# Optimization experiments

Hardware: AMD Instinct MI355X
Metric: run time of the kernel (lower is better)

Reference implementation:

```python
import jax, jax.numpy as jnp
import numpy as np

B, L, DM = 32, 64, 512
NODES = 16            # patch_size -> graph nodes
NODE_DIM = 10
CONV_CH, SKIP_CH = 32, 32
GDEP = 2
ALPHA = 0.05
D_STATE, D_CONV = 16, 4
D_INNER = 2 * DM      # Mamba expand=2
DT_RANK = DM // 16    # 32
K = DM - NODES + 1    # start_conv kernel height = 497


def setup_inputs() -> dict:
    key = jax.random.key(0)
    ks = jax.random.split(key, 16)
    n = jax.random.normal
    inp = {
        "x": n(ks[0], (B, L, DM), jnp.float32),
        "nodevec1": n(ks[1], (NODES, NODE_DIM), jnp.float32),
        "nodevec2": n(ks[2], (NODE_DIM, NODES), jnp.float32),
        "start_w": n(ks[3], (CONV_CH, K), jnp.float32) * 0.02,
        "start_b": jnp.zeros((CONV_CH,), jnp.float32),
        "mix_w": n(ks[4], (SKIP_CH, (GDEP + 1) * CONV_CH), jnp.float32) * 0.05,
        "mix_b": jnp.zeros((SKIP_CH,), jnp.float32),
        "end_w": n(ks[5], (L, SKIP_CH, L), jnp.float32) * 0.02,
        "end_b": jnp.zeros((L,), jnp.float32),
        "lin_w": n(ks[6], (DM, NODES), jnp.float32) * 0.05,
        "lin_b": jnp.zeros((DM,), jnp.float32),
        "gnorm_g": jnp.ones((DM,), jnp.float32),
        "gnorm_b": jnp.zeros((DM,), jnp.float32),
        "in_proj_w": n(ks[7], (2 * D_INNER, DM), jnp.float32) * 0.02,
        "conv_w": n(ks[8], (D_INNER, D_CONV), jnp.float32) * 0.2,
        "conv_b": jnp.zeros((D_INNER,), jnp.float32),
        "xproj_w": n(ks[9], (DT_RANK + 2 * D_STATE, D_INNER), jnp.float32) * 0.02,
        "dtproj_w": n(ks[10], (D_INNER, DT_RANK), jnp.float32) * 0.05,
        "dtproj_b": n(ks[11], (D_INNER,), jnp.float32) * 0.05,
        "A_log": jnp.log(jnp.tile(jnp.arange(1, D_STATE + 1, dtype=jnp.float32), (D_INNER, 1))),
        "Dp": jnp.ones((D_INNER,), jnp.float32),
        "out_proj_w": n(ks[12], (DM, D_INNER), jnp.float32) * 0.02,
        "norm_g": jnp.ones((DM,), jnp.float32),
        "norm_b": jnp.zeros((DM,), jnp.float32),
    }
    return inp


def layer_norm(x, g, b, eps=1e-5):
    mu = x.mean(-1, keepdims=True)
    var = ((x - mu) ** 2).mean(-1, keepdims=True)
    return (x - mu) / jnp.sqrt(var + eps) * g + b


def graph_block(x, nodevec1, nodevec2, start_w, start_b, mix_w, mix_b,
                end_w, end_b, lin_w, lin_b, gnorm_g, gnorm_b):
    # adaptive adjacency over the NODES=16 graph nodes
    adp = jax.nn.softmax(jax.nn.relu(nodevec1 @ nodevec2), axis=1)
    # start_conv: Conv2d(1, CONV_CH, (DM-NODES+1, 1)) on [B,1,DM,L]
    xi = jnp.swapaxes(x, 1, 2)  # [B, DM, L]
    windows = jnp.stack([xi[:, i:i + K, :] for i in range(NODES)], axis=1)  # [B, NODES, K, L]
    h0 = jnp.einsum('bikl,ck->bcil', windows, start_w) + start_b[None, :, None, None]  # [B,CONV_CH,NODES,L]
    # mixprop graph conv
    adj = adp + jnp.eye(NODES, dtype=x.dtype)
    a = adj / adj.sum(axis=1, keepdims=True)
    h = h0
    outs = [h]
    for _ in range(GDEP):
        h = ALPHA * h0 + (1.0 - ALPHA) * jnp.einsum('bcwl,vw->bcvl', h, a)
        outs.append(h)
    ho = jnp.concatenate(outs, axis=1)  # [B, (GDEP+1)*CONV_CH, NODES, L]
    ho = jnp.einsum('bcil,oc->boil', ho, mix_w) + mix_b[None, :, None, None]  # 1x1 conv mlp
    ho = jax.nn.gelu(ho, approximate=False)
    # end_conv: Conv2d(SKIP_CH, L, (1, L)) -> [B, L, NODES]
    out = jnp.einsum('bcil,ocl->boi', ho, end_w) + end_b[None, :, None]
    out = out @ lin_w.T + lin_b  # [B, L, DM]
    return layer_norm(x + out, gnorm_g, gnorm_b)


def mamba(x, in_proj_w, conv_w, conv_b, xproj_w, dtproj_w, dtproj_b,
          A_log, Dp, out_proj_w):
    xz = x @ in_proj_w.T                       # [B,L,2*D_INNER]
    xin, z = jnp.split(xz, 2, axis=-1)
    # causal depthwise conv1d
    xt = jnp.swapaxes(xin, 1, 2)               # [B, D_INNER, L]
    xp = jnp.pad(xt, ((0, 0), (0, 0), (D_CONV - 1, 0)))
    xc = sum(xp[:, :, k:k + L] * conv_w[None, :, k, None] for k in range(D_CONV))
    xc = xc + conv_b[None, :, None]
    xc = jax.nn.silu(jnp.swapaxes(xc, 1, 2))   # [B, L, D_INNER]
    x_dbl = xc @ xproj_w.T
    dt, Bm, Cm = jnp.split(x_dbl, [DT_RANK, DT_RANK + D_STATE], axis=-1)
    dt = jax.nn.softplus(dt @ dtproj_w.T + dtproj_b)      # [B,L,D_INNER]
    A = -jnp.exp(A_log)                                    # [D_INNER, D_STATE]
    dA = jnp.exp(dt[..., None] * A)                        # [B,L,D_INNER,D_STATE]
    dBu = dt[..., None] * Bm[:, :, None, :] * xc[..., None]

    def step(h, inputs):
        dA_t, dBu_t, C_t = inputs
        h = dA_t * h + dBu_t                               # [B,D_INNER,D_STATE]
        y = jnp.einsum('bds,bs->bd', h, C_t)
        return h, y

    h0 = jnp.zeros((B, D_INNER, D_STATE), dtype=x.dtype)
    _, ys = jax.lax.scan(step, h0, (jnp.swapaxes(dA, 0, 1),
                                    jnp.swapaxes(dBu, 0, 1),
                                    jnp.swapaxes(Cm, 0, 1)))
    y = jnp.swapaxes(ys, 0, 1) + xc * Dp                   # skip term D*u
    y = y * jax.nn.silu(z)
    return y @ out_proj_w.T


def reference(x, nodevec1, nodevec2, start_w, start_b, mix_w, mix_b, end_w, end_b,
              lin_w, lin_b, gnorm_g, gnorm_b, in_proj_w, conv_w, conv_b, xproj_w,
              dtproj_w, dtproj_b, A_log, Dp, out_proj_w, norm_g, norm_b):
    xg = graph_block(x, nodevec1, nodevec2, start_w, start_b, mix_w, mix_b,
                     end_w, end_b, lin_w, lin_b, gnorm_g, gnorm_b)
    out = layer_norm(mamba(xg, in_proj_w, conv_w, conv_b, xproj_w, dtproj_w,
                           dtproj_b, A_log, Dp, out_proj_w), norm_g, norm_b)
    out = jax.nn.gelu(out, approximate=False)
    return out + xg
```

## Files before the change

### kernel.cpp

```cpp
#include <hip/hip_runtime.h>
#include <hip/hip_bf16.h>
#include <math.h>

typedef __hip_bfloat16 bf16;
typedef __attribute__((ext_vector_type(8))) short short8;
typedef __attribute__((ext_vector_type(4))) float f32x4;

#define B_ 32
#define L_ 64
#define DM_ 512
#define NODES_ 16
#define KW_ 497
#define DIN_ 1024

__device__ __forceinline__ float b2f(bf16 x){ return __bfloat162float(x); }
__device__ __forceinline__ bf16 f2b(float x){ return __float2bfloat16(x); }
__device__ __forceinline__ float us2f(unsigned short u){ return __uint_as_float(((unsigned)u)<<16); }
__device__ __forceinline__ float geluf(float x){ return 0.5f*x*(1.0f+erff(x*0.70710678118654752f)); }
__device__ __forceinline__ float siluf(float x){ return x/(1.0f+__expf(-x)); }

__global__ void __launch_bounds__(256) k_prep(const float* ew, bf16* ewt, const float* win, bf16* wbin,
                       const float* wo, bf16* wob, const float* xw, bf16* xwb,
                       const float* dw, float* dwt, const float* x, bf16* xbf,
                       const float* sw, bf16* SwT,
                       const float* nv1, const float* nv2,
                       const float* mw, const float* mb, const float* sb,
                       bf16* Q, float* bcomp){
  int bid = blockIdx.x;
  int tid = threadIdx.x;
  if (bid < 512){
    int idx = bid*256 + tid;
    int o = idx >> 11, j = idx & 2047;
    int c = j & 31, l = j >> 5;
    ewt[idx] = f2b(ew[o*2048 + c*64 + l]);
  } else if (bid < 4608){
    int idx = (bid-512)*256 + tid;
    wbin[idx] = f2b(win[idx]);
  } else if (bid < 6656){
    int idx = (bid-4608)*256 + tid;
    wob[idx] = f2b(wo[idx]);
  } else if (bid < 6912){
    int idx = (bid-6656)*256 + tid;
    xwb[idx] = f2b(xw[idx]);
  } else if (bid < 7040){
    int k = (bid-6912)*256 + tid;
    dwt[k] = dw[(k & 1023)*32 + (k >> 10)];
  } else if (bid < 11136){
    int idx = (bid-7040)*256 + tid;
    xbf[idx] = f2b(x[idx]);
  } else if (bid < 12160){
    int idx = (bid-11136)*256 + tid;
    int k = idx >> 9, m = idx & 511;
    int c = m >> 4, w = m & 15;
    int kk = k - w;
    SwT[idx] = f2b((kk >= 0 && kk < KW_) ? sw[c*KW_ + kk] : 0.f);
  } else {
    __shared__ float as[256], M1[256], M2[256], mws[32*96], sbs[32], bo[32];
    int qb = bid - 12160;
    for (int t=tid; t<32*96; t+=256) mws[t]=mw[t];
    if (tid<32) sbs[tid]=sb[tid];
    __syncthreads();
    if (tid<16){
      int i=tid;
      float row[16];
      for(int j=0;j<16;j++){ float s=0.f; for(int k=0;k<10;k++) s+=nv1[i*10+k]*nv2[k*16+j]; row[j]=fmaxf(s,0.f); }
      float m=row[0]; for(int j=1;j<16;j++) m=fmaxf(m,row[j]);
      float den=0.f; for(int j=0;j<16;j++){row[j]=__expf(row[j]-m); den+=row[j];}
      for(int j=0;j<16;j++) row[j]/=den;
      row[i]+=1.f;
      float rs=0.f; for(int j=0;j<16;j++) rs+=row[j];
      float inv=1.f/rs;
      for(int j=0;j<16;j++) as[i*16+j]=row[j]*inv;
    }
    __syncthreads();
    { int i=tid>>4, w=tid&15;
      M1[tid] = 0.05f*((i==w)?1.f:0.f) + 0.95f*as[i*16+w]; }
    __syncthreads();
    { int i=tid>>4, w=tid&15;
      float s=0.f;
      for(int u=0;u<16;u++) s+=as[i*16+u]*M1[u*16+w];
      M2[tid] = 0.05f*((i==w)?1.f:0.f) + 0.95f*s; }
    if (tid<32){
      float s=mb[tid];
      for(int c=0;c<32;c++) s += (mws[tid*96+c]+mws[tid*96+32+c]+mws[tid*96+64+c])*sbs[c];
      bo[tid]=s;
    }
    __syncthreads();
    if (qb == 0){
      for (int n=tid; n<512; n+=256) bcomp[n] = bo[n&31];
    }
    int base = qb*4096;
    for (int t=tid; t<4096; t+=256){
      int idx = base + t;
      int n=idx>>9, m=idx&511;
      int i=n>>5, o=n&31, c=m>>4, w=m&15;
      float v = mws[o*96+c]*((i==w)?1.f:0.f)
              + mws[o*96+32+c]*M1[i*16+w]
              + mws[o*96+64+c]*M2[i*16+w];
      Q[idx]=f2b(v);
    }
  }
}

__global__ void __launch_bounds__(256) k_gemmU(const ushort* A, int lda,
                                               const ushort* W, int ldw,
                                               int K, bf16* C, int ldc,
                                               const float* bias, int act){
  __shared__ ushort As[128*56] __attribute__((aligned(16)));
  __shared__ ushort Ws[128*56] __attribute__((aligned(16)));
  int tid = threadIdx.x;
  int m0 = blockIdx.y*128, n0 = blockIdx.x*128;
  int lane = tid & 63, wave = tid >> 6;
  int wm = (wave>>1)*64, wn = (wave&1)*64;
  int l15 = lane & 15, quad = lane >> 4;
  f32x4 acc[4][4];
  #pragma unroll
  for (int mi=0;mi<4;mi++)
    #pragma unroll
    for (int ni=0;ni<4;ni++) acc[mi][ni] = (f32x4){0.f,0.f,0.f,0.f};
  for (int k0 = 0; k0 < K; k0 += 32){
    __syncthreads();
    #pragma unroll
    for (int p=0;p<2;p++){
      int idx = p*256 + tid;
      int row = idx>>2, ch = idx&3;
      *(uint4*)&As[row*56 + ch*8] = *(const uint4*)(A + (size_t)(m0+row)*lda + k0 + ch*8);
      *(uint4*)&Ws[row*56 + ch*8] = *(const uint4*)(W + (size_t)(n0+row)*ldw + k0 + ch*8);
    }
    __syncthreads();
    short8 af[4], bfr[4];
    #pragma unroll
    for (int mi=0;mi<4;mi++) af[mi] = *(const short8*)&As[(wm+mi*16+l15)*56 + quad*8];
    #pragma unroll
    for (int ni=0;ni<4;ni++) bfr[ni] = *(const short8*)&Ws[(wn+ni*16+l15)*56 + quad*8];
    #pragma unroll
    for (int mi=0;mi<4;mi++)
      #pragma unroll
      for (int ni=0;ni<4;ni++)
        acc[mi][ni] = __builtin_amdgcn_mfma_f32_16x16x32_bf16(af[mi], bfr[ni], acc[mi][ni], 0, 0, 0);
  }
  #pragma unroll
  for (int mi=0;mi<4;mi++){
    #pragma unroll
    for (int ni=0;ni<4;ni++){
      int col = n0 + wn + ni*16 + l15;
      float bs = (act==1) ? bias[col] : 0.f;
      #pragma unroll
      for (int r=0;r<4;r++){
        int row = m0 + wm + mi*16 + quad*4 + r;
        float v = acc[mi][ni][r];
        if (act==1) v = geluf(v + bs);
        C[(size_t)row*ldc + col] = f2b(v);
      }
    }
  }
}

__global__ void __launch_bounds__(256) k_gemmC(const ushort* A, const ushort* W,
                                               const float* cw, const float* cb,
                                               bf16* xcb, bf16* zb){
  __shared__ ushort smem[16896] __attribute__((aligned(16)));
  ushort* As = smem;
  ushort* Ws = smem + 7168;
  int tid = threadIdx.x;
  int m0 = blockIdx.y*128, n0 = blockIdx.x*128;
  int lane = tid & 63, wave = tid >> 6;
  int wm = (wave>>1)*64, wn = (wave&1)*64;
  int l15 = lane & 15, quad = lane >> 4;
  f32x4 acc[4][4];
  #pragma unroll
  for (int mi=0;mi<4;mi++)
    #pragma unroll
    for (int ni=0;ni<4;ni++) acc[mi][ni] = (f32x4){0.f,0.f,0.f,0.f};
  for (int k0 = 0; k0 < 512; k0 += 32){
    __syncthreads();
    #pragma unroll
    for (int p=0;p<2;p++){
      int idx = p*256 + tid;
      int row = idx>>2, ch = idx&3;
      *(uint4*)&As[row*56 + ch*8] = *(const uint4*)(A + (size_t)(m0+row)*512 + k0 + ch*8);
      *(uint4*)&Ws[row*56 + ch*8] = *(const uint4*)(W + (size_t)(n0+row)*512 + k0 + ch*8);
    }
    __syncthreads();
    short8 af[4], bfr[4];
    #pragma unroll
    for (int mi=0;mi<4;mi++) af[mi] = *(const short8*)&As[(wm+mi*16+l15)*56 + quad*8];
    #pragma unroll
    for (int ni=0;ni<4;ni++) bfr[ni] = *(const short8*)&Ws[(wn+ni*16+l15)*56 + quad*8];
    #pragma unroll
    for (int mi=0;mi<4;mi++)
      #pragma unroll
      for (int ni=0;ni<4;ni++)
        acc[mi][ni] = __builtin_amdgcn_mfma_f32_16x16x32_bf16(af[mi], bfr[ni], acc[mi][ni], 0, 0, 0);
  }
  if (n0 >= 1024){
    #pragma unroll
    for (int mi=0;mi<4;mi++){
      #pragma unroll
      for (int ni=0;ni<4;ni++){
        int col = n0 - 1024 + wn + ni*16 + l15;
        #pragma unroll
        for (int r=0;r<4;r++){
          int row = m0 + wm + mi*16 + quad*4 + r;
          zb[(size_t)row*1024 + col] = f2b(acc[mi][ni][r]);
        }
      }
    }
    return;
  }
  __syncthreads();
  ushort* st = smem + wave*4224;
  #pragma unroll
  for (int mi=0;mi<4;mi++){
    #pragma unroll
    for (int ni=0;ni<4;ni++){
      #pragma unroll
      for (int r=0;r<4;r++){
        bf16 v = f2b(acc[mi][ni][r]);
        st[(mi*16+quad*4+r)*66 + ni*16+l15] = *(unsigned short*)&v;
      }
    }
  }
  __syncthreads();
  int j = n0 + wn + lane;
  float w0 = cw[j*4+0], w1 = cw[j*4+1], w2 = cw[j*4+2], w3 = cw[j*4+3];
  float cbj = cb[j];
  float p0=0.f, p1=0.f, p2=0.f;
  int rowbase = m0 + wm;
  for (int rr=0; rr<64; rr++){
    float xv = us2f(st[rr*66 + lane]);
    float v = cbj + w0*p0 + w1*p1 + w2*p2 + w3*xv;
    xcb[(size_t)(rowbase+rr)*1024 + j] = f2b(siluf(v));
    p0 = p1; p1 = p2; p2 = xv;
  }
}

__global__ void __launch_bounds__(256) k_xprojM(const ushort* A, const ushort* W,
                                                float* xdl, float* BC){
  __shared__ ushort As[64*56] __attribute__((aligned(16)));
  __shared__ ushort Ws[64*56] __attribute__((aligned(16)));
  int tid = threadIdx.x;
  int m0 = blockIdx.y*64;
  int lane = tid & 63, wave = tid >> 6;
  int wm = (wave>>1)*32, wn = (wave&1)*32;
  int l15 = lane & 15, quad = lane >> 4;
  f32x4 acc[2][2];
  #pragma unroll
  for (int mi=0;mi<2;mi++)
    #pragma unroll
    for (int ni=0;ni<2;ni++) acc[mi][ni] = (f32x4){0.f,0.f,0.f,0.f};
  for (int k0 = 0; k0 < 1024; k0 += 32){
    __syncthreads();
    int row = tid>>2, ch = tid&3;
    *(uint4*)&As[row*56 + ch*8] = *(const uint4*)(A + (size_t)(m0+row)*1024 + k0 + ch*8);
    *(uint4*)&Ws[row*56 + ch*8] = *(const uint4*)(W + (size_t)row*1024 + k0 + ch*8);
    __syncthreads();
    short8 af[2], bfr[2];
    #pragma unroll
    for (int mi=0;mi<2;mi++) af[mi] = *(const short8*)&As[(wm+mi*16+l15)*56 + quad*8];
    #pragma unroll
    for (int ni=0;ni<2;ni++) bfr[ni] = *(const short8*)&Ws[(wn+ni*16+l15)*56 + quad*8];
    #pragma unroll
    for (int mi=0;mi<2;mi++)
      #pragma unroll
      for (int ni=0;ni<2;ni++)
        acc[mi][ni] = __builtin_amdgcn_mfma_f32_16x16x32_bf16(af[mi], bfr[ni], acc[mi][ni], 0, 0, 0);
  }
  #pragma unroll
  for (int mi=0;mi<2;mi++){
    #pragma unroll
    for (int ni=0;ni<2;ni++){
      int col = wn + ni*16 + l15;
      #pragma unroll
      for (int r=0;r<4;r++){
        int row = m0 + wm + mi*16 + quad*4 + r;
        float v = acc[mi][ni][r];
        if (col < 32) xdl[row*32 + col] = v;
        else          BC[row*32 + (col-32)] = v;
      }
    }
  }
}

__global__ void k_endconv(const bf16* mixed, const bf16* ewt, const float* eb, float* eout){
  __shared__ float ms[2048];
  __shared__ float psum[64][4];
  int bi = blockIdx.x;
  int b = bi >> 4, i = bi & 15;
  int tid = threadIdx.x;
  {
    int t0 = tid*8;
    int l = t0 >> 5, cc0 = t0 & 31;
    short8 v = *(const short8*)(mixed + (size_t)(b*64+l)*512 + i*32 + cc0);
    #pragma unroll
    for (int k=0;k<8;k++) ms[t0+k] = us2f((unsigned short)v[k]);
  }
  __syncthreads();
  int o = tid >> 2, q = tid & 3;
  const short8* er8 = (const short8*)(ewt + (size_t)o*2048 + q*512);
  const float* mr = ms + q*512;
  float p0 = 0.f, p1 = 0.f;
  for (int j8=0;j8<64;j8++){
    short8 w8 = er8[j8];
    const float* mq = mr + j8*8;
    p0 += mq[0]*us2f((unsigned short)w8[0]) + mq[1]*us2f((unsigned short)w8[1])
        + mq[2]*us2f((unsigned short)w8[2]) + mq[3]*us2f((unsigned short)w8[3]);
    p1 += mq[4]*us2f((unsigned short)w8[4]) + mq[5]*us2f((unsigned short)w8[5])
        + mq[6]*us2f((unsigned short)w8[6]) + mq[7]*us2f((unsigned short)w8[7]);
  }
  psum[o][q] = p0 + p1;
  __syncthreads();
  if (tid < 64){
    float s = psum[tid][0]+psum[tid][1]+psum[tid][2]+psum[tid][3] + eb[tid];
    eout[(b*64+tid)*16 + i] = s;
  }
}

__global__ void __launch_bounds__(512) k_linln(const float* eout, const float* x, const float* lw, const float* lb,
                        const float* gg, const float* gb, bf16* xgb){
  __shared__ float es[16];
  __shared__ float red[8];
  int tok = blockIdx.x;
  int tid = threadIdx.x;
  if (tid < 16) es[tid] = eout[tok*16 + tid];
  __syncthreads();
  float v = x[tok*512+tid] + lb[tid];
  for (int i=0;i<16;i++) v += es[i]*lw[tid*16+i];
  float s = v;
  for (int off=32; off; off>>=1) s += __shfl_down(s, off, 64);
  int wv = tid>>6, ln = tid&63;
  if (ln==0) red[wv] = s;
  __syncthreads();
  if (tid==0){ float t=0.f; for(int w=0;w<8;w++) t+=red[w]; red[0]=t; }
  __syncthreads();
  float mean = red[0] * (1.f/512.f);
  __syncthreads();
  float d = v - mean;
  float s2 = d*d;
  for (int off=32; off; off>>=1) s2 += __shfl_down(s2, off, 64);
  if (ln==0) red[wv] = s2;
  __syncthreads();
  if (tid==0){ float t=0.f; for(int w=0;w<8;w++) t+=red[w]; red[0]=t; }
  __syncthreads();
  float rstd = rsqrtf(red[0]*(1.f/512.f) + 1e-5f);
  xgb[tok*512+tid] = f2b(d*rstd*gg[tid] + gb[tid]);
}

__global__ void __launch_bounds__(256) k_gemm64(const ushort* A, int lda,
                                                const ushort* W, int ldw,
                                                int K, char* Cb){
  __shared__ ushort As[64*56] __attribute__((aligned(16)));
  __shared__ ushort Ws[64*56] __attribute__((aligned(16)));
  int tid = threadIdx.x;
  int m0 = blockIdx.y*64, n0 = blockIdx.x*64;
  int lane = tid & 63, wave = tid >> 6;
  int wm = (wave>>1)*32, wn = (wave&1)*32;
  int l15 = lane & 15, quad = lane >> 4;
  f32x4 acc[2][2];
  #pragma unroll
  for (int mi=0;mi<2;mi++)
    #pragma unroll
    for (int ni=0;ni<2;ni++) acc[mi][ni] = (f32x4){0.f,0.f,0.f,0.f};
  for (int k0 = 0; k0 < K; k0 += 32){
    __syncthreads();
    int row = tid>>2, ch = tid&3;
    *(uint4*)&As[row*56 + ch*8] = *(const uint4*)(A + (size_t)(m0+row)*lda + k0 + ch*8);
    *(uint4*)&Ws[row*56 + ch*8] = *(const uint4*)(W + (size_t)(n0+row)*ldw + k0 + ch*8);
    __syncthreads();
    short8 af[2], bfr[2];
    #pragma unroll
    for (int mi=0;mi<2;mi++) af[mi] = *(const short8*)&As[(wm+mi*16+l15)*56 + quad*8];
    #pragma unroll
    for (int ni=0;ni<2;ni++) bfr[ni] = *(const short8*)&Ws[(wn+ni*16+l15)*56 + quad*8];
    #pragma unroll
    for (int mi=0;mi<2;mi++)
      #pragma unroll
      for (int ni=0;ni<2;ni++)
        acc[mi][ni] = __builtin_amdgcn_mfma_f32_16x16x32_bf16(af[mi], bfr[ni], acc[mi][ni], 0, 0, 0);
  }
  #pragma unroll
  for (int mi=0;mi<2;mi++){
    #pragma unroll
    for (int ni=0;ni<2;ni++){
      int col = n0 + wn + ni*16 + l15;
      #pragma unroll
      for (int r=0;r<4;r++){
        int row = m0 + wm + mi*16 + quad*4 + r;
        *(float*)(Cb + (size_t)row*4096 + col*4) = acc[mi][ni][r];
      }
    }
  }
}

__global__ void __launch_bounds__(128) k_scan5(const float* xdl, const float* BCg,
                       const float* dwt, const float* db, const float* Dp,
                       const bf16* zb, bf16* xcb){
  __shared__ float bcs[2048];
  __shared__ float xds[2048];
  __shared__ unsigned short xcl[8192];
  __shared__ unsigned short zl[8192];
  int tid = threadIdx.x;
  int b = blockIdx.x >> 3, q = blockIdx.x & 7;
  int d = q*128 + tid;
  for (int t=tid; t<2048; t+=128){ bcs[t] = BCg[b*2048+t]; xds[t] = xdl[b*2048+t]; }
  for (int t=tid; t<8192; t+=128){
    int l = t >> 7, dl = t & 127;
    xcl[t] = ((const unsigned short*)xcb)[(size_t)(b*64+l)*1024 + q*128 + dl];
    zl[t]  = ((const unsigned short*)zb)[(size_t)(b*64+l)*1024 + q*128 + dl];
  }
  float myw[32];
  #pragma unroll
  for (int qq=0;qq<32;qq++) myw[qq] = dwt[qq*1024 + d];
  float dbv = db[d];
  float Dd = Dp[d];
  __syncthreads();
  float h[16];
  #pragma unroll
  for (int s=0;s<16;s++) h[s]=0.f;
  for (int l=0;l<64;l++){
    const float* xr = xds + l*32;
    float a0=dbv, a1=0.f, a2=0.f, a3=0.f;
    #pragma unroll
    for (int j=0;j<8;j++){
      a0 += xr[j]     *myw[j];
      a1 += xr[8+j]   *myw[8+j];
      a2 += xr[16+j]  *myw[16+j];
      a3 += xr[24+j]  *myw[24+j];
    }
    float dtv = (a0+a1)+(a2+a3);
    if (dtv <= 20.f) dtv = __logf(1.f + __expf(dtv));
    float xcv = us2f(xcl[l*128 + tid]);
    float dx = dtv*xcv;
    float e1 = __expf(-dtv);
    float e2 = e1*e1, e4 = e2*e2, e8 = e4*e4;
    float dA[16];
    dA[0]=e1;       dA[1]=e2;       dA[2]=e2*e1;     dA[3]=e4;
    dA[4]=e4*e1;    dA[5]=e4*e2;    dA[6]=e4*dA[2];  dA[7]=e8;
    dA[8]=e8*e1;    dA[9]=e8*e2;    dA[10]=e8*dA[2]; dA[11]=e8*e4;
    dA[12]=e8*dA[4];dA[13]=e8*dA[5];dA[14]=e8*dA[6]; dA[15]=e8*e8;
    const float* bl = bcs + l*32;
    float y0=0.f,y1=0.f,y2=0.f,y3=0.f;
    #pragma unroll
    for (int s=0;s<16;s+=4){
      h[s]   = dA[s]  *h[s]   + dx*bl[s];    y0 += h[s]  *bl[16+s];
      h[s+1] = dA[s+1]*h[s+1] + dx*bl[s+1];  y1 += h[s+1]*bl[17+s];
      h[s+2] = dA[s+2]*h[s+2] + dx*bl[s+2];  y2 += h[s+2]*bl[18+s];
      h[s+3] = dA[s+3]*h[s+3] + dx*bl[s+3];  y3 += h[s+3]*bl[19+s];
    }
    float y = (y0+y1)+(y2+y3);
    float zv = us2f(zl[l*128 + tid]);
    xcb[(size_t)(b*64+l)*1024 + d] = f2b((y + xcv*Dd) * siluf(zv));
  }
}

__global__ void __launch_bounds__(512) k_outfin(const char* ypb, const bf16* xgb,
                        const float* ng, const float* nb, float* out){
  __shared__ float red[8];
  int tok = blockIdx.x, tid = threadIdx.x;
  const float* yr = (const float*)(ypb + (size_t)tok*4096);
  float v = yr[tid];
  float s = v;
  for (int off=32; off; off>>=1) s += __shfl_down(s, off, 64);
  int wv = tid>>6, ln = tid&63;
  if (ln==0) red[wv] = s;
  __syncthreads();
  if (tid==0){ float t=0.f; for(int w=0;w<8;w++) t+=red[w]; red[0]=t; }
  __syncthreads();
  float mean = red[0] * (1.f/512.f);
  __syncthreads();
  float d = v - mean;
  float s2 = d*d;
  for (int off=32; off; off>>=1) s2 += __shfl_down(s2, off, 64);
  if (ln==0) red[wv] = s2;
  __syncthreads();
  if (tid==0){ float t=0.f; for(int w=0;w<8;w++) t+=red[w]; red[0]=t; }
  __syncthreads();
  float rstd = rsqrtf(red[0]*(1.f/512.f) + 1e-5f);
  out[tok*512+tid] = geluf(d*rstd*ng[tid] + nb[tid]) + b2f(xgb[tok*512+tid]);
}

extern "C" void kernel_launch(void* const* d_in, const int* in_sizes, int n_in,
                              void* d_out, int out_size, void* d_ws, size_t ws_size,
                              hipStream_t stream) {
  (void)in_sizes; (void)n_in; (void)out_size; (void)ws_size;
  const float* x        = (const float*)d_in[0];
  const float* nv1      = (const float*)d_in[1];
  const float* nv2      = (const float*)d_in[2];
  const float* start_w  = (const float*)d_in[3];
  const float* start_b  = (const float*)d_in[4];
  const float* mix_w    = (const float*)d_in[5];
  const float* mix_b    = (const float*)d_in[6];
  const float* end_w    = (const float*)d_in[7];
  const float* end_b    = (const float*)d_in[8];
  const float* lin_w    = (const float*)d_in[9];
  const float* lin_b    = (const float*)d_in[10];
  const float* gnorm_g  = (const float*)d_in[11];
  const float* gnorm_b  = (const float*)d_in[12];
  const float* in_proj_w= (const float*)d_in[13];
  const float* conv_w   = (const float*)d_in[14];
  const float* conv_b   = (const float*)d_in[15];
  const float* xproj_w  = (const float*)d_in[16];
  const float* dtproj_w = (const float*)d_in[17];
  const float* dtproj_b = (const float*)d_in[18];
  const float* Dp       = (const float*)d_in[20];
  const float* out_proj_w=(const float*)d_in[21];
  const float* norm_g   = (const float*)d_in[22];
  const float* norm_b   = (const float*)d_in[23];
  float* out = (float*)d_out;

  char* wsb = (char*)d_ws;
  bf16*  xgb   = (bf16*) (wsb + 0);
  bf16*  Wbin  = (bf16*) (wsb + (2u<<20));
  bf16*  Wob   = (bf16*) (wsb + (4u<<20));
  bf16*  xwb   = (bf16*) (wsb + (5u<<20));
  float* dwt   = (float*)(wsb + (5u<<20) + 262144);
  float* xdl   = (float*)(wsb + (6u<<20));
  float* BC    = (float*)(wsb + (6u<<20) + 262144);
  float* eout  = (float*)(wsb + (7u<<20) + 4096);
  bf16*  ewt   = (bf16*) (wsb + (7u<<20) + 262144);
  bf16*  hm    = (bf16*) (wsb + (8u<<20));
  bf16*  zb    = (bf16*) (wsb + (10u<<20));
  bf16*  xcb   = (bf16*) (wsb + (18u<<20));
  char*  yp    =         (wsb + (22u<<20));
  bf16*  xbf   = (bf16*) (wsb + (30u<<20));
  bf16*  SwT   = (bf16*) (wsb + (32u<<20));
  bf16*  Q     = (bf16*) (wsb + (33u<<20));
  bf16*  Wcomp = (bf16*) (wsb + (34u<<20));
  float* bcomp = (float*)(wsb + (35u<<20));

  k_prep  <<<12224, 256, 0, stream>>>(end_w, ewt, in_proj_w, Wbin, out_proj_w, Wob,
                                      xproj_w, xwb, dtproj_w, dwt, x, xbf, start_w, SwT,
                                      nv1, nv2, mix_w, mix_b, start_b, Q, bcomp);
  k_gemmU <<<dim3(4,4),  256, 0, stream>>>((const ushort*)Q, 512, (const ushort*)SwT, 512,
                                           512, Wcomp, 512, (const float*)0, 0);
  k_gemmU <<<dim3(4,16), 256, 0, stream>>>((const ushort*)xbf, 512, (const ushort*)Wcomp, 512,
                                           512, hm, 512, bcomp, 1);
  k_endconv<<<512,  256, 0, stream>>>(hm, ewt, end_b, eout);
  k_linln  <<<2048, 512, 0, stream>>>(eout, x, lin_w, lin_b, gnorm_g, gnorm_b, xgb);
  k_gemmC  <<<dim3(16,16), 256, 0, stream>>>((const ushort*)xgb, (const ushort*)Wbin,
                                             conv_w, conv_b, xcb, zb);
  k_xprojM <<<dim3(1,32), 256, 0, stream>>>((const ushort*)xcb, (const ushort*)xwb, xdl, BC);
  k_scan5  <<<256,  128, 0, stream>>>(xdl, BC, dwt, dtproj_b, Dp, zb, xcb);
  k_gemm64 <<<dim3(8,32), 256, 0, stream>>>((const ushort*)xcb, 1024,
                                            (const ushort*)Wob, 1024,
                                            1024, yp);
  k_outfin <<<2048, 512, 0, stream>>>(yp, xgb, norm_g, norm_b, out);
}
```

Measured before the change: 262.2 us.

## Vectorize prep, fuse endconv into linln, split-K xproj, two-thread-per-channel scan

The prep kernel now converts four elements per thread with vector loads and stores, so it launches far fewer blocks. The end-conv reduction is fused into the linear+layernorm kernel, which removes one launch and the eout round trip. The x-projection GEMM is split four ways along K to fill more CUs, and the scan kernel sums the four partials on load. The scan also splits each channel's 16 states across two threads joined by shuffles, doubling parallelism at the cost of extra shuffles and redundant partial-sum reads.

```diff
diff --git a/kernel.cpp b/kernel.cpp
--- a/kernel.cpp
+++ b/kernel.cpp
@@ -5,6 +5,7 @@
 typedef __hip_bfloat16 bf16;
 typedef __attribute__((ext_vector_type(8))) short short8;
 typedef __attribute__((ext_vector_type(4))) float f32x4;
+typedef __attribute__((ext_vector_type(4))) unsigned short ushort4v;
 
 #define B_ 32
 #define L_ 64
@@ -15,6 +16,7 @@
 
 __device__ __forceinline__ float b2f(bf16 x){ return __bfloat162float(x); }
 __device__ __forceinline__ bf16 f2b(float x){ return __float2bfloat16(x); }
+__device__ __forceinline__ unsigned short f2bu(float x){ bf16 t = __float2bfloat16(x); return *reinterpret_cast<unsigned short*>(&t); }
 __device__ __forceinline__ float us2f(unsigned short u){ return __uint_as_float(((unsigned)u)<<16); }
 __device__ __forceinline__ float geluf(float x){ return 0.5f*x*(1.0f+erff(x*0.70710678118654752f)); }
 __device__ __forceinline__ float siluf(float x){ return x/(1.0f+__expf(-x)); }
@@ -28,35 +30,64 @@
                        bf16* Q, float* bcomp){
   int bid = blockIdx.x;
   int tid = threadIdx.x;
-  if (bid < 512){
-    int idx = bid*256 + tid;
+  if (bid < 128){
+    int idx = (bid*256 + tid)*4;
     int o = idx >> 11, j = idx & 2047;
     int c = j & 31, l = j >> 5;
-    ewt[idx] = f2b(ew[o*2048 + c*64 + l]);
-  } else if (bid < 4608){
-    int idx = (bid-512)*256 + tid;
-    wbin[idx] = f2b(win[idx]);
-  } else if (bid < 6656){
-    int idx = (bid-4608)*256 + tid;
-    wob[idx] = f2b(wo[idx]);
-  } else if (bid < 6912){
-    int idx = (bid-6656)*256 + tid;
-    xwb[idx] = f2b(xw[idx]);
-  } else if (bid < 7040){
-    int k = (bid-6912)*256 + tid;
-    dwt[k] = dw[(k & 1023)*32 + (k >> 10)];
-  } else if (bid < 11136){
-    int idx = (bid-7040)*256 + tid;
-    xbf[idx] = f2b(x[idx]);
-  } else if (bid < 12160){
-    int idx = (bid-11136)*256 + tid;
+    const float* src = ew + o*2048 + c*64 + l;
+    ushort4v v;
+    #pragma unroll
+    for (int k=0;k<4;k++) v[k] = f2bu(src[k*64]);
+    *(ushort4v*)&ewt[idx] = v;
+  } else if (bid < 1152){
+    int idx = ((bid-128)*256 + tid)*4;
+    f32x4 s = *(const f32x4*)(win+idx);
+    ushort4v v;
+    #pragma unroll
+    for (int k=0;k<4;k++) v[k] = f2bu(s[k]);
+    *(ushort4v*)&wbin[idx] = v;
+  } else if (bid < 1664){
+    int idx = ((bid-1152)*256 + tid)*4;
+    f32x4 s = *(const f32x4*)(wo+idx);
+    ushort4v v;
+    #pragma unroll
+    for (int k=0;k<4;k++) v[k] = f2bu(s[k]);
+    *(ushort4v*)&wob[idx] = v;
+  } else if (bid < 1728){
+    int idx = ((bid-1664)*256 + tid)*4;
+    f32x4 s = *(const f32x4*)(xw+idx);
+    ushort4v v;
+    #pragma unroll
+    for (int k=0;k<4;k++) v[k] = f2bu(s[k]);
+    *(ushort4v*)&xwb[idx] = v;
+  } else if (bid < 1760){
+    int k0 = ((bid-1728)*256 + tid)*4;
+    f32x4 v;
+    #pragma unroll
+    for (int k=0;k<4;k++) v[k] = dw[((k0+k) & 1023)*32 + ((k0+k) >> 10)];
+    *(f32x4*)&dwt[k0] = v;
+  } else if (bid < 2784){
+    int idx = ((bid-1760)*256 + tid)*4;
+    f32x4 s = *(const f32x4*)(x+idx);
+    ushort4v v;
+    #pragma unroll
+    for (int k=0;k<4;k++) v[k] = f2bu(s[k]);
+    *(ushort4v*)&xbf[idx] = v;
+  } else if (bid < 3040){
+    int idx = ((bid-2784)*256 + tid)*4;
     int k = idx >> 9, m = idx & 511;
-    int c = m >> 4, w = m & 15;
-    int kk = k - w;
-    SwT[idx] = f2b((kk >= 0 && kk < KW_) ? sw[c*KW_ + kk] : 0.f);
+    int c = m >> 4;
+    ushort4v v;
+    #pragma unroll
+    for (int t=0;t<4;t++){
+      int w = (m+t) & 15;
+      int kk = k - w;
+      v[t] = f2bu((kk >= 0 && kk < KW_) ? sw[c*KW_ + kk] : 0.f);
+    }
+    *(ushort4v*)&SwT[idx] = v;
   } else {
     __shared__ float as[256], M1[256], M2[256], mws[32*96], sbs[32], bo[32];
-    int qb = bid - 12160;
+    int qb = bid - 3040;
     for (int t=tid; t<32*96; t+=256) mws[t]=mw[t];
     if (tid<32) sbs[tid]=sb[tid];
     __syncthreads();
@@ -235,12 +266,14 @@
   }
 }
 
-__global__ void __launch_bounds__(256) k_xprojM(const ushort* A, const ushort* W,
-                                                float* xdl, float* BC){
+__global__ void __launch_bounds__(256) k_xprojM2(const ushort* A, const ushort* W,
+                                                 float* xdlp, float* BCp){
   __shared__ ushort As[64*56] __attribute__((aligned(16)));
   __shared__ ushort Ws[64*56] __attribute__((aligned(16)));
   int tid = threadIdx.x;
   int m0 = blockIdx.y*64;
+  int kk = blockIdx.x;
+  int kbase = kk*256;
   int lane = tid & 63, wave = tid >> 6;
   int wm = (wave>>1)*32, wn = (wave&1)*32;
   int l15 = lane & 15, quad = lane >> 4;
@@ -249,7 +282,7 @@
   for (int mi=0;mi<2;mi++)
     #pragma unroll
     for (int ni=0;ni<2;ni++) acc[mi][ni] = (f32x4){0.f,0.f,0.f,0.f};
-  for (int k0 = 0; k0 < 1024; k0 += 32){
+  for (int k0 = kbase; k0 < kbase+256; k0 += 32){
     __syncthreads();
     int row = tid>>2, ch = tid&3;
     *(uint4*)&As[row*56 + ch*8] = *(const uint4*)(A + (size_t)(m0+row)*1024 + k0 + ch*8);
@@ -266,6 +299,8 @@
       for (int ni=0;ni<2;ni++)
         acc[mi][ni] = __builtin_amdgcn_mfma_f32_16x16x32_bf16(af[mi], bfr[ni], acc[mi][ni], 0, 0, 0);
   }
+  float* xo = xdlp + (size_t)kk*65536;
+  float* bo = BCp  + (size_t)kk*65536;
   #pragma unroll
   for (int mi=0;mi<2;mi++){
     #pragma unroll
@@ -275,56 +310,47 @@
       for (int r=0;r<4;r++){
         int row = m0 + wm + mi*16 + quad*4 + r;
         float v = acc[mi][ni][r];
-        if (col < 32) xdl[row*32 + col] = v;
-        else          BC[row*32 + (col-32)] = v;
+        if (col < 32) xo[row*32 + col] = v;
+        else          bo[row*32 + (col-32)] = v;
       }
     }
   }
 }
 
-__global__ void k_endconv(const bf16* mixed, const bf16* ewt, const float* eb, float* eout){
-  __shared__ float ms[2048];
-  __shared__ float psum[64][4];
-  int bi = blockIdx.x;
-  int b = bi >> 4, i = bi & 15;
-  int tid = threadIdx.x;
-  {
-    int t0 = tid*8;
-    int l = t0 >> 5, cc0 = t0 & 31;
-    short8 v = *(const short8*)(mixed + (size_t)(b*64+l)*512 + i*32 + cc0);
-    #pragma unroll
-    for (int k=0;k<8;k++) ms[t0+k] = us2f((unsigned short)v[k]);
-  }
-  __syncthreads();
-  int o = tid >> 2, q = tid & 3;
-  const short8* er8 = (const short8*)(ewt + (size_t)o*2048 + q*512);
-  const float* mr = ms + q*512;
-  float p0 = 0.f, p1 = 0.f;
-  for (int j8=0;j8<64;j8++){
-    short8 w8 = er8[j8];
-    const float* mq = mr + j8*8;
-    p0 += mq[0]*us2f((unsigned short)w8[0]) + mq[1]*us2f((unsigned short)w8[1])
-        + mq[2]*us2f((unsigned short)w8[2]) + mq[3]*us2f((unsigned short)w8[3]);
-    p1 += mq[4]*us2f((unsigned short)w8[4]) + mq[5]*us2f((unsigned short)w8[5])
-        + mq[6]*us2f((unsigned short)w8[6]) + mq[7]*us2f((unsigned short)w8[7]);
-  }
-  psum[o][q] = p0 + p1;
-  __syncthreads();
-  if (tid < 64){
-    float s = psum[tid][0]+psum[tid][1]+psum[tid][2]+psum[tid][3] + eb[tid];
-    eout[(b*64+tid)*16 + i] = s;
-  }
-}
-
-__global__ void __launch_bounds__(512) k_linln(const float* eout, const float* x, const float* lw, const float* lb,
+__global__ void __launch_bounds__(512) k_linln2(const bf16* mixed, const bf16* ewt, const float* eb,
+                        const float* x, const float* lw, const float* lb,
                         const float* gg, const float* gb, bf16* xgb){
   __shared__ float es[16];
   __shared__ float red[8];
   int tok = blockIdx.x;
-  int tid = threadIdx.x;
-  if (tid < 16) es[tid] = eout[tok*16 + tid];
+  int b = tok >> 6, o = tok & 63;
+  int tid = threadIdx.x;
+  {
+    int i = tid >> 5, s = tid & 31;
+    const ushort* mrow = (const ushort*)mixed + (size_t)b*32768 + i*32;
+    const ushort* erow = (const ushort*)ewt + (size_t)o*2048 + s*64;
+    float acc = 0.f;
+    #pragma unroll
+    for (int half=0; half<2; half++){
+      int l = s*2 + half;
+      const ushort* mp = mrow + (size_t)l*512;
+      const ushort* ep = erow + half*32;
+      #pragma unroll
+      for (int c=0;c<32;c+=8){
+        short8 mv = *(const short8*)(mp + c);
+        short8 ev = *(const short8*)(ep + c);
+        #pragma unroll
+        for (int k=0;k<8;k++)
+          acc += us2f((unsigned short)mv[k]) * us2f((unsigned short)ev[k]);
+      }
+    }
+    #pragma unroll
+    for (int off=16; off; off>>=1) acc += __shfl_xor(acc, off, 64);
+    if (s == 0) es[i] = acc + eb[o];
+  }
   __syncthreads();
   float v = x[tok*512+tid] + lb[tid];
+  #pragma unroll
   for (int i=0;i<16;i++) v += es[i]*lw[tid*16+i];
   float s = v;
   for (int off=32; off; off>>=1) s += __shfl_down(s, off, 64);
@@ -392,7 +418,7 @@
   }
 }
 
-__global__ void __launch_bounds__(128) k_scan5(const float* xdl, const float* BCg,
+__global__ void __launch_bounds__(256) k_scan6(const float* xdlp, const float* BCp,
                        const float* dwt, const float* db, const float* Dp,
                        const bf16* zb, bf16* xcb){
   __shared__ float bcs[2048];
@@ -401,55 +427,60 @@
   __shared__ unsigned short zl[8192];
   int tid = threadIdx.x;
   int b = blockIdx.x >> 3, q = blockIdx.x & 7;
-  int d = q*128 + tid;
-  for (int t=tid; t<2048; t+=128){ bcs[t] = BCg[b*2048+t]; xds[t] = xdl[b*2048+t]; }
-  for (int t=tid; t<8192; t+=128){
+  int ch = tid >> 1, p = tid & 1;
+  int d = q*128 + ch;
+  for (int t=tid; t<2048; t+=256){
+    int off = b*2048 + t;
+    xds[t] = xdlp[off] + xdlp[65536+off] + xdlp[131072+off] + xdlp[196608+off];
+    bcs[t] = BCp[off]  + BCp[65536+off]  + BCp[131072+off]  + BCp[196608+off];
+  }
+  for (int t=tid; t<8192; t+=256){
     int l = t >> 7, dl = t & 127;
     xcl[t] = ((const unsigned short*)xcb)[(size_t)(b*64+l)*1024 + q*128 + dl];
     zl[t]  = ((const unsigned short*)zb)[(size_t)(b*64+l)*1024 + q*128 + dl];
   }
-  float myw[32];
-  #pragma unroll
-  for (int qq=0;qq<32;qq++) myw[qq] = dwt[qq*1024 + d];
+  float myw[16];
+  #pragma unroll
+  for (int jj=0;jj<16;jj++) myw[jj] = dwt[(p*16+jj)*1024 + d];
   float dbv = db[d];
   float Dd = Dp[d];
   __syncthreads();
-  float h[16];
-  #pragma unroll
-  for (int s=0;s<16;s++) h[s]=0.f;
+  float h[8];
+  #pragma unroll
+  for (int s=0;s<8;s++) h[s]=0.f;
   for (int l=0;l<64;l++){
-    const float* xr = xds + l*32;
-    float a0=dbv, a1=0.f, a2=0.f, a3=0.f;
+    const float* xr = xds + l*32 + p*16;
+    float a0=0.f, a1=0.f;
     #pragma unroll
     for (int j=0;j<8;j++){
-      a0 += xr[j]     *myw[j];
-      a1 += xr[8+j]   *myw[8+j];
-      a2 += xr[16+j]  *myw[16+j];
-      a3 += xr[24+j]  *myw[24+j];
-    }
-    float dtv = (a0+a1)+(a2+a3);
-    if (dtv <= 20.f) dtv = __logf(1.f + __expf(dtv));
-    float xcv = us2f(xcl[l*128 + tid]);
+      a0 += xr[j]   * myw[j];
+      a1 += xr[8+j] * myw[8+j];
+    }
+    float part = a0 + a1;
+    float raw = part + __shfl_xor(part, 1, 64) + dbv;
+    float er = __expf(raw);
+    float dtv = (raw > 20.f) ? raw : __logf(1.f + er);
+    float e1 = 1.f/(1.f + er);
+    float xcv = us2f(xcl[l*128 + ch]);
     float dx = dtv*xcv;
-    float e1 = __expf(-dtv);
-    float e2 = e1*e1, e4 = e2*e2, e8 = e4*e4;
-    float dA[16];
-    dA[0]=e1;       dA[1]=e2;       dA[2]=e2*e1;     dA[3]=e4;
-    dA[4]=e4*e1;    dA[5]=e4*e2;    dA[6]=e4*dA[2];  dA[7]=e8;
-    dA[8]=e8*e1;    dA[9]=e8*e2;    dA[10]=e8*dA[2]; dA[11]=e8*e4;
-    dA[12]=e8*dA[4];dA[13]=e8*dA[5];dA[14]=e8*dA[6]; dA[15]=e8*e8;
-    const float* bl = bcs + l*32;
-    float y0=0.f,y1=0.f,y2=0.f,y3=0.f;
-    #pragma unroll
-    for (int s=0;s<16;s+=4){
-      h[s]   = dA[s]  *h[s]   + dx*bl[s];    y0 += h[s]  *bl[16+s];
-      h[s+1] = dA[s+1]*h[s+1] + dx*bl[s+1];  y1 += h[s+1]*bl[17+s];
-      h[s+2] = dA[s+2]*h[s+2] + dx*bl[s+2];  y2 += h[s+2]*bl[18+s];
-      h[s+3] = dA[s+3]*h[s+3] + dx*bl[s+3];  y3 += h[s+3]*bl[19+s];
-    }
-    float y = (y0+y1)+(y2+y3);
-    float zv = us2f(zl[l*128 + tid]);
-    xcb[(size_t)(b*64+l)*1024 + d] = f2b((y + xcv*Dd) * siluf(zv));
+    float e2=e1*e1, e3=e2*e1, e4=e2*e2, e5=e4*e1, e6=e4*e2, e7=e4*e3, e8=e4*e4;
+    float pw[8] = {e1,e2,e3,e4,e5,e6,e7,e8};
+    float base = p ? e8 : 1.0f;
+    const float* bl = bcs + l*32 + p*8;
+    const float* cl = bcs + l*32 + 16 + p*8;
+    float y0=0.f, y1=0.f;
+    #pragma unroll
+    for (int k=0;k<8;k+=2){
+      float dA0 = pw[k]*base, dA1 = pw[k+1]*base;
+      h[k]   = dA0*h[k]   + dx*bl[k];    y0 += h[k]  *cl[k];
+      h[k+1] = dA1*h[k+1] + dx*bl[k+1];  y1 += h[k+1]*cl[k+1];
+    }
+    float y = y0 + y1;
+    y += __shfl_xor(y, 1, 64);
+    if (p == 0){
+      float zv = us2f(zl[l*128 + ch]);
+      xcb[(size_t)(b*64+l)*1024 + d] = f2b((y + xcv*Dd) * siluf(zv));
+    }
   }
 }
 
@@ -514,9 +545,6 @@
   bf16*  Wob   = (bf16*) (wsb + (4u<<20));
   bf16*  xwb   = (bf16*) (wsb + (5u<<20));
   float* dwt   = (float*)(wsb + (5u<<20) + 262144);
-  float* xdl   = (float*)(wsb + (6u<<20));
-  float* BC    = (float*)(wsb + (6u<<20) + 262144);
-  float* eout  = (float*)(wsb + (7u<<20) + 4096);
   bf16*  ewt   = (bf16*) (wsb + (7u<<20) + 262144);
   bf16*  hm    = (bf16*) (wsb + (8u<<20));
   bf16*  zb    = (bf16*) (wsb + (10u<<20));
@@ -527,20 +555,21 @@
   bf16*  Q     = (bf16*) (wsb + (33u<<20));
   bf16*  Wcomp = (bf16*) (wsb + (34u<<20));
   float* bcomp = (float*)(wsb + (35u<<20));
-
-  k_prep  <<<12224, 256, 0, stream>>>(end_w, ewt, in_proj_w, Wbin, out_proj_w, Wob,
-                                      xproj_w, xwb, dtproj_w, dwt, x, xbf, start_w, SwT,
-                                      nv1, nv2, mix_w, mix_b, start_b, Q, bcomp);
+  float* xdlp  = (float*)(wsb + (40u<<20));
+  float* BCp   = (float*)(wsb + (41u<<20));
+
+  k_prep  <<<3104, 256, 0, stream>>>(end_w, ewt, in_proj_w, Wbin, out_proj_w, Wob,
+                                     xproj_w, xwb, dtproj_w, dwt, x, xbf, start_w, SwT,
+                                     nv1, nv2, mix_w, mix_b, start_b, Q, bcomp);
   k_gemmU <<<dim3(4,4),  256, 0, stream>>>((const ushort*)Q, 512, (const ushort*)SwT, 512,
                                            512, Wcomp, 512, (const float*)0, 0);
   k_gemmU <<<dim3(4,16), 256, 0, stream>>>((const ushort*)xbf, 512, (const ushort*)Wcomp, 512,
                                            512, hm, 512, bcomp, 1);
-  k_endconv<<<512,  256, 0, stream>>>(hm, ewt, end_b, eout);
-  k_linln  <<<2048, 512, 0, stream>>>(eout, x, lin_w, lin_b, gnorm_g, gnorm_b, xgb);
+  k_linln2 <<<2048, 512, 0, stream>>>(hm, ewt, end_b, x, lin_w, lin_b, gnorm_g, gnorm_b, xgb);
   k_gemmC  <<<dim3(16,16), 256, 0, stream>>>((const ushort*)xgb, (const ushort*)Wbin,
                                              conv_w, conv_b, xcb, zb);
-  k_xprojM <<<dim3(1,32), 256, 0, stream>>>((const ushort*)xcb, (const ushort*)xwb, xdl, BC);
-  k_scan5  <<<256,  128, 0, stream>>>(xdl, BC, dwt, dtproj_b, Dp, zb, xcb);
+  k_xprojM2<<<dim3(4,32), 256, 0, stream>>>((const ushort*)xcb, (const ushort*)xwb, xdlp, BCp);
+  k_scan6  <<<256,  256, 0, stream>>>(xdlp, BCp, dwt, dtproj_b, Dp, zb, xcb);
   k_gemm64 <<<dim3(8,32), 256, 0, stream>>>((const ushort*)xcb, 1024,
                                             (const ushort*)Wob, 1024,
                                             1024, yp);
```

Result: no change. 264.7 us (+1.0%).
